# Kernel optimization log

Hardware: AMD Instinct MI355X
Metric: run time of the kernel (lower is better)

The kernel has to match this reference:

```python
import jax, jax.numpy as jnp
import numpy as np

CE_TEMP = 1.0
SIMW_TEMP = 0.1
NSEG = 2048
EPS = 1e-8
NEG = jnp.float32(-1e30)


def setup_inputs() -> dict:
    key = jax.random.key(0)
    k1, k2, k3, k4, k5, k6 = jax.random.split(key, 6)
    N, C, H, W, Ch, S = 2, 19, 128, 128, 256, NSEG
    inputs_plbl = jax.random.normal(k1, (N, C, H, W), dtype=jnp.float32)
    feats_plbl = jax.random.normal(k2, (N, Ch, H, W), dtype=jnp.float32)
    inputs = jax.random.normal(k3, (N, C, H, W), dtype=jnp.float32)
    # multi-hot targets per superpixel; ~2.3 active classes on average -> many multi-hot rows
    targets = jax.random.bernoulli(k4, 0.12, (N, S, C)).astype(jnp.float32)
    superpixels = jax.random.randint(k5, (N, H, W), 0, S, dtype=jnp.int32)
    spmasks = jax.random.bernoulli(k6, 0.5, (N, H, W))
    return {"inputs_plbl": inputs_plbl, "feats_plbl": feats_plbl, "inputs": inputs,
            "targets": targets, "superpixels": superpixels, "spmasks": spmasks}


def _per_image(out_plbl, feat, out, trg_table, sp, mask):
    # out_plbl: [HW,C] softmax'd pseudo-label probs; feat: [HW,Ch]; out: [HW,C];
    # trg_table: [S,C] multi-hot; sp: [HW] int superpixel ids; mask: [HW] bool
    HW, C = out_plbl.shape
    S = trg_table.shape[0]
    trg_pix = trg_table[sp]                                  # [HW,C]
    multi_spx = trg_table.sum(-1) > 1.0                      # [S]
    valid = mask & multi_spx[sp]                             # == spmask & multi-hot mask

    # scatter_max: argmax pixel per (superpixel, class) among valid pixels
    scores = jnp.where(valid[:, None], out_plbl, NEG)
    seg_max = jax.ops.segment_max(scores, sp, num_segments=S)       # [S,C]
    is_max = valid[:, None] & (scores >= seg_max[sp])
    cand = jnp.where(is_max, jnp.arange(HW, dtype=jnp.int32)[:, None], HW)
    proto_idx = jax.ops.segment_min(cand, sp, num_segments=S)       # [S,C]
    proto_idx = jnp.clip(proto_idx, 0, HW - 1)

    # prototype features and per-pixel similarities to own-superpixel class prototypes
    proto_feat = feat[proto_idx]                             # [S,C,Ch]
    pf_pix = proto_feat[sp]                                  # [HW,C,Ch] (dominant intermediate)
    sim = jnp.einsum('kcd,kd->kc', pf_pix, feat) / SIMW_TEMP  # [HW,C]

    # scatter_softmax over the active classes of the pixel's superpixel
    active = trg_pix > 0.0
    w_multi = jax.nn.softmax(jnp.where(active, sim, NEG), axis=-1)
    w_row = jnp.where(active, w_multi, trg_pix)              # inactive entries keep 0
    w = jnp.where(valid[:, None], w_row, trg_pix)            # non-multi pixels keep one-hot
    w = jax.lax.stop_gradient(w)                             # original computes weights under no_grad

    ce = -jnp.log(out + EPS)                                 # [HW,C]
    contrib = jnp.where(mask[:, None], w * ce, 0.0)
    any_valid = jnp.any(valid)                               # image skipped if no multi-hot masked pixel
    loss_i = jnp.where(any_valid, contrib.sum(), 0.0)
    cnt_i = jnp.where(any_valid, mask.sum(), 0)
    return loss_i, cnt_i


def reference(inputs_plbl, feats_plbl, inputs, targets, superpixels, spmasks):
    N, C, H, W = inputs_plbl.shape
    Ch = feats_plbl.shape[1]
    out_plbl = jax.nn.softmax(inputs_plbl / CE_TEMP, axis=1).transpose(0, 2, 3, 1).reshape(N, -1, C)
    feats = feats_plbl.transpose(0, 2, 3, 1).reshape(N, -1, Ch)
    out = jax.nn.softmax(inputs / CE_TEMP, axis=1).transpose(0, 2, 3, 1).reshape(N, -1, C)
    sp = superpixels.reshape(N, -1)
    mask = spmasks.reshape(N, -1)
    loss_i, cnt_i = jax.vmap(_per_image)(out_plbl, feats, out, targets, sp, mask)
    total = loss_i.sum()
    cnt = cnt_i.sum()
    return jnp.where(cnt > 0, total / jnp.maximum(cnt, 1).astype(jnp.float32), 0.0)
```

## Files before the change

kernel.cpp:

```cpp
#include <hip/hip_runtime.h>
#include <cstdint>
#include <cstddef>

#define NN   2
#define CC   19
#define HWD  16384
#define CH   256
#define SS   2048
#define BCAP 32

#define MAIN_BLKS  (2 * NN * HWD / 256)
#define TRAN_BLKS  ((HWD / 64) * (CH / 64) * NN)

#define OFF_SPCNT  622592
#define OFF_CNT    638976
#define OFF_VCNT   638984
#define OFF_SLOTS  638992
#define ZERO_F4    40001
#define OFF_ACT    640016
#define OFF_BUCKET 656400
#define OFF_CE     918544
#define OFF_FEAT   3408912

__device__ __forceinline__ unsigned short f2bf(float x) {
    unsigned u = __float_as_uint(x);
    return (unsigned short)((u + 0x7FFFu + ((u >> 16) & 1u)) >> 16);
}
__device__ __forceinline__ float bf2f(unsigned short h) {
    return __uint_as_float(((unsigned)h) << 16);
}

__global__ __launch_bounds__(256) void k_init(const float* __restrict__ trg,
                                              unsigned* __restrict__ actmask,
                                              float4* __restrict__ zb) {
    int tid = blockIdx.x * 256 + threadIdx.x;
    float4 z = make_float4(0.f, 0.f, 0.f, 0.f);
    for (int i = tid; i < ZERO_F4; i += 64 * 256) zb[i] = z;
    if (tid < NN * SS) {
        const float* t = trg + (size_t)tid * CC;
        unsigned mk = 0;
        int na = 0;
        #pragma unroll
        for (int c = 0; c < CC; ++c) {
            if (t[c] > 0.f) { mk |= (1u << c); ++na; }
        }
        if (na > 1) mk |= 0x80000000u;
        actmask[tid] = mk;
    }
}

__global__ __launch_bounds__(256) void k_fused(
        const float* __restrict__ xp, const float* __restrict__ xi,
        const float* __restrict__ F, const unsigned* __restrict__ actmask,
        const int* __restrict__ sp, const int* __restrict__ msk,
        int* __restrict__ sp_cnt, unsigned short* __restrict__ bucket,
        unsigned long long* __restrict__ amax,
        float* __restrict__ ce_pm, unsigned short* __restrict__ feat_t,
        int* __restrict__ cnt, int* __restrict__ vcnt, float* __restrict__ slots) {
    __shared__ float tile[64][65];
    __shared__ unsigned char vld[64];

    if (blockIdx.x < MAIN_BLKS) {
        int gid = blockIdx.x * blockDim.x + threadIdx.x;
        int partB = (gid >= NN * HWD);
        int idx = partB ? gid - NN * HWD : gid;
        int n = idx >> 14;
        int k = idx & (HWD - 1);
        int lane = threadIdx.x & 63;
        int m = (msk[idx] != 0);
        int s = sp[idx];
        unsigned flag = m ? actmask[(n << 11) + s] : 0u;
        int mu = (int)(flag >> 31);
        int valid = m && mu;

        if (!partB) {
            unsigned long long mb = __ballot(m);
            unsigned long long vb = __ballot(valid);
            if (valid) {
                int cell = (n << 11) + s;
                int pos = atomicAdd(&sp_cnt[cell], 1);
                if (pos < BCAP) bucket[(size_t)cell * BCAP + pos] = (unsigned short)k;
                const float* a = xp + (size_t)n * CC * HWD + k;
                float v[CC];
                float mx = -1e30f;
                #pragma unroll
                for (int c = 0; c < CC; ++c) { v[c] = a[(size_t)c * HWD]; mx = fmaxf(mx, v[c]); }
                float su = 0.f;
                #pragma unroll
                for (int c = 0; c < CC; ++c) { v[c] = expf(v[c] - mx); su += v[c]; }
                float inv = 1.f / su;
                unsigned long long low = (unsigned long long)(unsigned)(HWD - k);
                unsigned long long* arow = amax + (size_t)cell * CC;
                #pragma unroll
                for (int c = 0; c < CC; ++c) {
                    unsigned long long key =
                        ((unsigned long long)__float_as_uint(v[c] * inv) << 32) | low;
                    atomicMax(&arow[c], key);
                }
            }
            if (lane == 0) {
                if (mb) atomicAdd(&cnt[n], __popcll(mb));
                if (vb) atomicAdd(&vcnt[n], __popcll(vb));
            }
        } else {
            float contrib = 0.f;
            if (m) {
                const float* b = xi + (size_t)n * CC * HWD + k;
                float v[CC];
                float mx = -1e30f;
                #pragma unroll
                for (int c = 0; c < CC; ++c) { v[c] = b[(size_t)c * HWD]; mx = fmaxf(mx, v[c]); }
                float su = 0.f;
                #pragma unroll
                for (int c = 0; c < CC; ++c) su += expf(v[c] - mx);
                float lsu = logf(su);
                if (mu) {
                    float* cp = ce_pm + (size_t)idx * CC;
                    #pragma unroll
                    for (int c = 0; c < CC; ++c) cp[c] = lsu - (v[c] - mx);
                } else {
                    #pragma unroll
                    for (int c = 0; c < CC; ++c)
                        if ((flag >> c) & 1u) contrib += lsu - (v[c] - mx);
                }
            }
            #pragma unroll
            for (int off = 32; off >= 1; off >>= 1) contrib += __shfl_xor(contrib, off);
            if (lane == 0 && contrib != 0.f)
                atomicAdd(&slots[n * 128 + ((idx >> 6) & 127)], contrib);
        }
    } else {
        int b2 = blockIdx.x - MAIN_BLKS;
        int k0 = (b2 & 255) * 64;
        int d0 = ((b2 >> 8) & 3) * 64;
        int n  = b2 >> 10;
        int tx = threadIdx.x & 63, ty = threadIdx.x >> 6;
        const float* src = F + (size_t)n * CH * HWD;
        unsigned short* dst = feat_t + (size_t)n * HWD * CH;

        if (ty == 0) {
            int pix = n * HWD + k0 + tx;
            int m = (msk[pix] != 0);
            int fl = 0;
            if (m) fl = (int)(actmask[(n << 11) + sp[pix]] >> 31);
            vld[tx] = (unsigned char)fl;
        }
        #pragma unroll
        for (int i = 0; i < 16; ++i) {
            int dd = ty + 4 * i;
            tile[dd][tx] = src[(size_t)(d0 + dd) * HWD + (k0 + tx)];
        }
        __syncthreads();
        #pragma unroll
        for (int i = 0; i < 16; ++i) {
            int kk = ty + 4 * i;
            if (vld[kk]) dst[(size_t)(k0 + kk) * CH + (d0 + tx)] = f2bf(tile[tx][kk]);
        }
    }
}

__global__ __launch_bounds__(256) void k_sim(
        const unsigned short* __restrict__ feat_t, const float* __restrict__ ce_pm,
        const unsigned long long* __restrict__ amax, const unsigned* __restrict__ actmask,
        const int* __restrict__ sp_cnt, const unsigned short* __restrict__ bucket,
        float* __restrict__ slots) {
    int lane = threadIdx.x & 63;
    int id = (blockIdx.x << 2) + (threadIdx.x >> 6);
    int cnt_c = sp_cnt[id];
    if (cnt_c == 0) return;
    cnt_c = min(cnt_c, BCAP);
    int n = id >> 11;
    unsigned act = actmask[id] & 0x7FFFFu;
    int nact = __popc(act);

    int myc = 0;
    {
        int seen = 0;
        #pragma unroll
        for (int c = 0; c < CC; ++c) {
            int b = (int)((act >> c) & 1u);
            if (b && seen == lane) myc = c;
            seen += b;
        }
    }
    int ppix = 0;
    if (lane < nact) {
        unsigned long long key = amax[(size_t)id * CC + myc];
        ppix = HWD - (int)(unsigned)(key & 0xFFFFFFFFull);
    }
    const unsigned short* Fb = feat_t + (size_t)n * HWD * CH;
    int mypix = (lane < cnt_c) ? (int)bucket[(size_t)id * BCAP + lane] : 0;
    float wcontrib = 0.f;

    if (nact <= 4) {
        int p0 = __shfl(ppix, 0), p1 = __shfl(ppix, 1);
        int p2 = __shfl(ppix, 2), p3 = __shfl(ppix, 3);
        ushort4 q0 = ((const ushort4*)(Fb + (size_t)p0 * CH))[lane];
        ushort4 q1 = ((const ushort4*)(Fb + (size_t)p1 * CH))[lane];
        ushort4 q2 = ((const ushort4*)(Fb + (size_t)p2 * CH))[lane];
        ushort4 q3 = ((const ushort4*)(Fb + (size_t)p3 * CH))[lane];
        float4 pf0 = make_float4(bf2f(q0.x), bf2f(q0.y), bf2f(q0.z), bf2f(q0.w));
        float4 pf1 = make_float4(bf2f(q1.x), bf2f(q1.y), bf2f(q1.z), bf2f(q1.w));
        float4 pf2 = make_float4(bf2f(q2.x), bf2f(q2.y), bf2f(q2.z), bf2f(q2.w));
        float4 pf3 = make_float4(bf2f(q3.x), bf2f(q3.y), bf2f(q3.z), bf2f(q3.w));

        int pix = __shfl(mypix, 0);
        ushort4 q = ((const ushort4*)(Fb + (size_t)pix * CH))[lane];
        float cen = (lane < nact) ? ce_pm[((size_t)(n * HWD + pix)) * CC + myc] : 0.f;
        for (int i = 0; i < cnt_c; ++i) {
            float4 f = make_float4(bf2f(q.x), bf2f(q.y), bf2f(q.z), bf2f(q.w));
            float ce = cen;
            if (i + 1 < cnt_c) {
                int pixn = __shfl(mypix, i + 1);
                q = ((const ushort4*)(Fb + (size_t)pixn * CH))[lane];
                cen = (lane < nact) ? ce_pm[((size_t)(n * HWD + pixn)) * CC + myc] : 0.f;
            }
            float d0 = f.x * pf0.x + f.y * pf0.y + f.z * pf0.z + f.w * pf0.w;
            float d1 = f.x * pf1.x + f.y * pf1.y + f.z * pf1.z + f.w * pf1.w;
            float d2 = f.x * pf2.x + f.y * pf2.y + f.z * pf2.z + f.w * pf2.w;
            float d3 = f.x * pf3.x + f.y * pf3.y + f.z * pf3.z + f.w * pf3.w;
            #pragma unroll
            for (int off = 32; off >= 1; off >>= 1) {
                d0 += __shfl_xor(d0, off);
                d1 += __shfl_xor(d1, off);
                d2 += __shfl_xor(d2, off);
                d3 += __shfl_xor(d3, off);
            }
            float dsel = (lane == 0) ? d0 : (lane == 1) ? d1 : (lane == 2) ? d2 : d3;
            float mysim = (lane < nact) ? dsel * 10.0f : -1e30f;
            float mx = fmaxf(mysim, __shfl_xor(mysim, 1));
            mx = fmaxf(mx, __shfl_xor(mx, 2));
            float e = (lane < nact) ? expf(mysim - mx) : 0.f;
            float se = e;
            se += __shfl_xor(se, 1);
            se += __shfl_xor(se, 2);
            float c1 = (e / se) * ce;
            c1 += __shfl_xor(c1, 1);
            c1 += __shfl_xor(c1, 2);
            wcontrib += c1;
        }
    } else {
        for (int i = 0; i < cnt_c; ++i) {
            int pix = __shfl(mypix, i);
            float ce = (lane < nact) ? ce_pm[((size_t)(n * HWD + pix)) * CC + myc] : 0.f;
            ushort4 q = ((const ushort4*)(Fb + (size_t)pix * CH))[lane];
            float4 f = make_float4(bf2f(q.x), bf2f(q.y), bf2f(q.z), bf2f(q.w));
            float mysim = -1e30f;
            for (int a0 = 0; a0 < nact; a0 += 4) {
                int p0 = __shfl(ppix, a0);
                int p1 = __shfl(ppix, a0 + 1);
                int p2 = __shfl(ppix, a0 + 2);
                int p3 = __shfl(ppix, a0 + 3);
                ushort4 q0 = ((const ushort4*)(Fb + (size_t)p0 * CH))[lane];
                ushort4 q1 = ((const ushort4*)(Fb + (size_t)p1 * CH))[lane];
                ushort4 q2 = ((const ushort4*)(Fb + (size_t)p2 * CH))[lane];
                ushort4 q3 = ((const ushort4*)(Fb + (size_t)p3 * CH))[lane];
                float4 pf0 = make_float4(bf2f(q0.x), bf2f(q0.y), bf2f(q0.z), bf2f(q0.w));
                float4 pf1 = make_float4(bf2f(q1.x), bf2f(q1.y), bf2f(q1.z), bf2f(q1.w));
                float4 pf2 = make_float4(bf2f(q2.x), bf2f(q2.y), bf2f(q2.z), bf2f(q2.w));
                float4 pf3 = make_float4(bf2f(q3.x), bf2f(q3.y), bf2f(q3.z), bf2f(q3.w));
                float d0 = f.x * pf0.x + f.y * pf0.y + f.z * pf0.z + f.w * pf0.w;
                float d1 = f.x * pf1.x + f.y * pf1.y + f.z * pf1.z + f.w * pf1.w;
                float d2 = f.x * pf2.x + f.y * pf2.y + f.z * pf2.z + f.w * pf2.w;
                float d3 = f.x * pf3.x + f.y * pf3.y + f.z * pf3.z + f.w * pf3.w;
                #pragma unroll
                for (int off = 32; off >= 1; off >>= 1) {
                    d0 += __shfl_xor(d0, off);
                    d1 += __shfl_xor(d1, off);
                    d2 += __shfl_xor(d2, off);
                    d3 += __shfl_xor(d3, off);
                }
                float dsel = (lane == a0) ? d0 : (lane == a0 + 1) ? d1
                           : (lane == a0 + 2) ? d2 : d3;
                if (lane >= a0 && lane < a0 + 4 && lane < nact) mysim = dsel * 10.0f;
            }
            float mx = mysim;
            #pragma unroll
            for (int off = 16; off >= 1; off >>= 1) mx = fmaxf(mx, __shfl_xor(mx, off));
            float e = (lane < nact) ? expf(mysim - mx) : 0.f;
            float se = e;
            #pragma unroll
            for (int off = 16; off >= 1; off >>= 1) se += __shfl_xor(se, off);
            float c1 = (e / se) * ce;
            #pragma unroll
            for (int off = 16; off >= 1; off >>= 1) c1 += __shfl_xor(c1, off);
            wcontrib += c1;
        }
    }
    if (lane == 0 && wcontrib != 0.f)
        atomicAdd(&slots[(n << 7) + (id & 127)], wcontrib);
}

__global__ void k_final(const float* __restrict__ slots, const int* __restrict__ cnt,
                        const int* __restrict__ vcnt, float* __restrict__ out) {
    __shared__ float red[2];
    int t = threadIdx.x;
    int w = t >> 6;
    int lane = t & 63;
    float v = slots[w * 128 + lane] + slots[w * 128 + lane + 64];
    #pragma unroll
    for (int off = 32; off >= 1; off >>= 1) v += __shfl_xor(v, off);
    if (lane == 0) red[w] = v;
    __syncthreads();
    if (t == 0) {
        float total = 0.f;
        int c = 0;
        for (int n = 0; n < NN; ++n)
            if (vcnt[n] > 0) { total += red[n]; c += cnt[n]; }
        out[0] = (c > 0) ? total / (float)c : 0.f;
    }
}

extern "C" void kernel_launch(void* const* d_in, const int* in_sizes, int n_in,
                              void* d_out, int out_size, void* d_ws, size_t ws_size,
                              hipStream_t stream) {
    const float* inputs_plbl = (const float*)d_in[0];
    const float* feats_plbl  = (const float*)d_in[1];
    const float* inputs      = (const float*)d_in[2];
    const float* targets     = (const float*)d_in[3];
    const int*   superpixels = (const int*)d_in[4];
    const int*   spmasks     = (const int*)d_in[5];
    float* out = (float*)d_out;

    char* ws = (char*)d_ws;
    unsigned long long* amax = (unsigned long long*)ws;
    int*   sp_cnt  = (int*)(ws + OFF_SPCNT);
    int*   cnt     = (int*)(ws + OFF_CNT);
    int*   vcnt    = (int*)(ws + OFF_VCNT);
    float* slots   = (float*)(ws + OFF_SLOTS);
    unsigned* actmask = (unsigned*)(ws + OFF_ACT);
    unsigned short* bucket = (unsigned short*)(ws + OFF_BUCKET);
    float* ce_pm   = (float*)(ws + OFF_CE);
    unsigned short* feat_t = (unsigned short*)(ws + OFF_FEAT);

    k_init<<<64, 256, 0, stream>>>(targets, actmask, (float4*)ws);
    k_fused<<<MAIN_BLKS + TRAN_BLKS, 256, 0, stream>>>(
        inputs_plbl, inputs, feats_plbl, actmask, superpixels, spmasks,
        sp_cnt, bucket, amax, ce_pm, feat_t, cnt, vcnt, slots);
    k_sim<<<NN * SS / 4, 256, 0, stream>>>(feat_t, ce_pm, amax, actmask,
                                           sp_cnt, bucket, slots);
    k_final<<<1, 128, 0, stream>>>(slots, cnt, vcnt, out);
}
```

Before: 130.0 us.

## Merge per-pixel softmax paths and vectorize feature transpose with packed bf16 stores

```diff
diff --git a/kernel.cpp b/kernel.cpp
--- a/kernel.cpp
+++ b/kernel.cpp
@@ -9,7 +9,7 @@
 #define SS   2048
 #define BCAP 32
 
-#define MAIN_BLKS  (2 * NN * HWD / 256)
+#define MAIN_BLKS  (NN * HWD / 256)
 #define TRAN_BLKS  ((HWD / 64) * (CH / 64) * NN)
 
 #define OFF_SPCNT  622592
@@ -29,13 +29,15 @@
 __device__ __forceinline__ float bf2f(unsigned short h) {
     return __uint_as_float(((unsigned)h) << 16);
 }
+__device__ __forceinline__ unsigned pk2bf(float a, float b) {
+    return (unsigned)f2bf(a) | ((unsigned)f2bf(b) << 16);
+}
 
 __global__ __launch_bounds__(256) void k_init(const float* __restrict__ trg,
                                               unsigned* __restrict__ actmask,
                                               float4* __restrict__ zb) {
     int tid = blockIdx.x * 256 + threadIdx.x;
-    float4 z = make_float4(0.f, 0.f, 0.f, 0.f);
-    for (int i = tid; i < ZERO_F4; i += 64 * 256) zb[i] = z;
+    if (tid < ZERO_F4) zb[tid] = make_float4(0.f, 0.f, 0.f, 0.f);
     if (tid < NN * SS) {
         const float* t = trg + (size_t)tid * CC;
         unsigned mk = 0;
@@ -61,9 +63,7 @@
     __shared__ unsigned char vld[64];
 
     if (blockIdx.x < MAIN_BLKS) {
-        int gid = blockIdx.x * blockDim.x + threadIdx.x;
-        int partB = (gid >= NN * HWD);
-        int idx = partB ? gid - NN * HWD : gid;
+        int idx = blockIdx.x * 256 + threadIdx.x;
         int n = idx >> 14;
         int k = idx & (HWD - 1);
         int lane = threadIdx.x & 63;
@@ -72,89 +72,107 @@
         unsigned flag = m ? actmask[(n << 11) + s] : 0u;
         int mu = (int)(flag >> 31);
         int valid = m && mu;
-
-        if (!partB) {
-            unsigned long long mb = __ballot(m);
-            unsigned long long vb = __ballot(valid);
-            if (valid) {
-                int cell = (n << 11) + s;
-                int pos = atomicAdd(&sp_cnt[cell], 1);
-                if (pos < BCAP) bucket[(size_t)cell * BCAP + pos] = (unsigned short)k;
-                const float* a = xp + (size_t)n * CC * HWD + k;
-                float v[CC];
-                float mx = -1e30f;
+        unsigned long long mb = __ballot(m);
+        unsigned long long vb = __ballot(valid);
+
+        if (valid) {
+            int cell = (n << 11) + s;
+            int pos = atomicAdd(&sp_cnt[cell], 1);
+            if (pos < BCAP) bucket[(size_t)cell * BCAP + pos] = (unsigned short)k;
+            const float* a = xp + (size_t)n * CC * HWD + k;
+            float v[CC];
+            float mx = -1e30f;
+            #pragma unroll
+            for (int c = 0; c < CC; ++c) { v[c] = a[(size_t)c * HWD]; mx = fmaxf(mx, v[c]); }
+            float su = 0.f;
+            #pragma unroll
+            for (int c = 0; c < CC; ++c) { v[c] = expf(v[c] - mx); su += v[c]; }
+            float inv = 1.f / su;
+            unsigned long long low = (unsigned long long)(unsigned)(HWD - k);
+            unsigned long long* arow = amax + (size_t)cell * CC;
+            #pragma unroll
+            for (int c = 0; c < CC; ++c) {
+                unsigned long long key =
+                    ((unsigned long long)__float_as_uint(v[c] * inv) << 32) | low;
+                atomicMax(&arow[c], key);
+            }
+        }
+        float contrib = 0.f;
+        if (m) {
+            const float* b = xi + (size_t)n * CC * HWD + k;
+            float v[CC];
+            float mx = -1e30f;
+            #pragma unroll
+            for (int c = 0; c < CC; ++c) { v[c] = b[(size_t)c * HWD]; mx = fmaxf(mx, v[c]); }
+            float su = 0.f;
+            #pragma unroll
+            for (int c = 0; c < CC; ++c) su += expf(v[c] - mx);
+            float lsu = logf(su);
+            if (mu) {
+                float* cp = ce_pm + (size_t)idx * CC;
                 #pragma unroll
-                for (int c = 0; c < CC; ++c) { v[c] = a[(size_t)c * HWD]; mx = fmaxf(mx, v[c]); }
-                float su = 0.f;
+                for (int c = 0; c < CC; ++c) cp[c] = lsu - (v[c] - mx);
+            } else {
                 #pragma unroll
-                for (int c = 0; c < CC; ++c) { v[c] = expf(v[c] - mx); su += v[c]; }
-                float inv = 1.f / su;
-                unsigned long long low = (unsigned long long)(unsigned)(HWD - k);
-                unsigned long long* arow = amax + (size_t)cell * CC;
-                #pragma unroll
-                for (int c = 0; c < CC; ++c) {
-                    unsigned long long key =
-                        ((unsigned long long)__float_as_uint(v[c] * inv) << 32) | low;
-                    atomicMax(&arow[c], key);
-                }
-            }
-            if (lane == 0) {
-                if (mb) atomicAdd(&cnt[n], __popcll(mb));
-                if (vb) atomicAdd(&vcnt[n], __popcll(vb));
-            }
-        } else {
-            float contrib = 0.f;
-            if (m) {
-                const float* b = xi + (size_t)n * CC * HWD + k;
-                float v[CC];
-                float mx = -1e30f;
-                #pragma unroll
-                for (int c = 0; c < CC; ++c) { v[c] = b[(size_t)c * HWD]; mx = fmaxf(mx, v[c]); }
-                float su = 0.f;
-                #pragma unroll
-                for (int c = 0; c < CC; ++c) su += expf(v[c] - mx);
-                float lsu = logf(su);
-                if (mu) {
-                    float* cp = ce_pm + (size_t)idx * CC;
-                    #pragma unroll
-                    for (int c = 0; c < CC; ++c) cp[c] = lsu - (v[c] - mx);
-                } else {
-                    #pragma unroll
-                    for (int c = 0; c < CC; ++c)
-                        if ((flag >> c) & 1u) contrib += lsu - (v[c] - mx);
-                }
-            }
-            #pragma unroll
-            for (int off = 32; off >= 1; off >>= 1) contrib += __shfl_xor(contrib, off);
-            if (lane == 0 && contrib != 0.f)
-                atomicAdd(&slots[n * 128 + ((idx >> 6) & 127)], contrib);
+                for (int c = 0; c < CC; ++c)
+                    if ((flag >> c) & 1u) contrib += lsu - (v[c] - mx);
+            }
+        }
+        #pragma unroll
+        for (int off = 32; off >= 1; off >>= 1) contrib += __shfl_xor(contrib, off);
+        if (lane == 0) {
+            if (contrib != 0.f) atomicAdd(&slots[n * 128 + ((idx >> 6) & 127)], contrib);
+            if (mb) atomicAdd(&cnt[n], __popcll(mb));
+            if (vb) atomicAdd(&vcnt[n], __popcll(vb));
         }
     } else {
         int b2 = blockIdx.x - MAIN_BLKS;
         int k0 = (b2 & 255) * 64;
         int d0 = ((b2 >> 8) & 3) * 64;
         int n  = b2 >> 10;
-        int tx = threadIdx.x & 63, ty = threadIdx.x >> 6;
+        int t  = threadIdx.x;
         const float* src = F + (size_t)n * CH * HWD;
         unsigned short* dst = feat_t + (size_t)n * HWD * CH;
 
-        if (ty == 0) {
-            int pix = n * HWD + k0 + tx;
+        if (t < 64) {
+            int pix = n * HWD + k0 + t;
             int m = (msk[pix] != 0);
             int fl = 0;
             if (m) fl = (int)(actmask[(n << 11) + sp[pix]] >> 31);
-            vld[tx] = (unsigned char)fl;
-        }
-        #pragma unroll
-        for (int i = 0; i < 16; ++i) {
-            int dd = ty + 4 * i;
-            tile[dd][tx] = src[(size_t)(d0 + dd) * HWD + (k0 + tx)];
+            vld[t] = (unsigned char)fl;
+        }
+        {
+            int u   = t & 15;
+            int dd0 = t >> 4;
+            #pragma unroll
+            for (int r = 0; r < 4; ++r) {
+                int dd = dd0 + 16 * r;
+                float4 f4 = *(const float4*)(src + (size_t)(d0 + dd) * HWD + (k0 + 4 * u));
+                tile[dd][4 * u + 0] = f4.x;
+                tile[dd][4 * u + 1] = f4.y;
+                tile[dd][4 * u + 2] = f4.z;
+                tile[dd][4 * u + 3] = f4.w;
+            }
         }
         __syncthreads();
-        #pragma unroll
-        for (int i = 0; i < 16; ++i) {
-            int kk = ty + 4 * i;
-            if (vld[kk]) dst[(size_t)(k0 + kk) * CH + (d0 + tx)] = f2bf(tile[tx][kk]);
+        {
+            int kk = t >> 2;
+            int q  = t & 3;
+            if (vld[kk]) {
+                uint4 w0, w1;
+                int cb = 16 * q;
+                w0.x = pk2bf(tile[cb + 0][kk], tile[cb + 1][kk]);
+                w0.y = pk2bf(tile[cb + 2][kk], tile[cb + 3][kk]);
+                w0.z = pk2bf(tile[cb + 4][kk], tile[cb + 5][kk]);
+                w0.w = pk2bf(tile[cb + 6][kk], tile[cb + 7][kk]);
+                w1.x = pk2bf(tile[cb + 8][kk], tile[cb + 9][kk]);
+                w1.y = pk2bf(tile[cb + 10][kk], tile[cb + 11][kk]);
+                w1.z = pk2bf(tile[cb + 12][kk], tile[cb + 13][kk]);
+                w1.w = pk2bf(tile[cb + 14][kk], tile[cb + 15][kk]);
+                uint4* dp = (uint4*)(dst + (size_t)(k0 + kk) * CH + d0 + cb);
+                dp[0] = w0;
+                dp[1] = w1;
+            }
         }
     }
 }
@@ -333,7 +351,7 @@
     float* ce_pm   = (float*)(ws + OFF_CE);
     unsigned short* feat_t = (unsigned short*)(ws + OFF_FEAT);
 
-    k_init<<<64, 256, 0, stream>>>(targets, actmask, (float4*)ws);
+    k_init<<<160, 256, 0, stream>>>(targets, actmask, (float4*)ws);
     k_fused<<<MAIN_BLKS + TRAN_BLKS, 256, 0, stream>>>(
         inputs_plbl, inputs, feats_plbl, actmask, superpixels, spmasks,
         sp_cnt, bucket, amax, ce_pm, feat_t, cnt, vcnt, slots);
```

New measurement: 133.4 us. 1.03x slower.
